# Kernel optimization log

Measured on AMD Instinct MI355X. Metric: run time of the kernel, lower is better.

## Reference

```python
import jax, jax.numpy as jnp
import numpy as np

N, E, D, L, G, C = 20000, 320000, 512, 6, 64, 10
EPS = 1e-5


def setup_inputs() -> dict:
    key = jax.random.key(0)
    ks = jax.random.split(key, 8)
    s = 0.05  # small init scale to keep activations sane across 6 layers
    x = jax.random.normal(ks[0], (N, D), jnp.float32)
    edge_index = jax.random.randint(ks[1], (2, E), 0, N, jnp.int32)
    batch = jnp.sort(jax.random.randint(ks[2], (N,), 0, G, jnp.int32))
    W_rel = jax.random.normal(ks[3], (L, D, D), jnp.float32) * s
    b_rel = jnp.zeros((L, D), jnp.float32)
    W_root = jax.random.normal(ks[4], (L, D, D), jnp.float32) * s
    gamma = jnp.ones((L, D), jnp.float32)
    beta = jnp.zeros((L, D), jnp.float32)
    lin_w = jax.random.normal(ks[5], (D, C), jnp.float32) * s
    lin_b = jnp.zeros((C,), jnp.float32)
    return {"x": x, "edge_index": edge_index, "batch": batch,
            "W_rel": W_rel, "b_rel": b_rel, "W_root": W_root,
            "gamma": gamma, "beta": beta, "lin_w": lin_w, "lin_b": lin_b}


def reference(x, edge_index, batch, W_rel, b_rel, W_root, gamma, beta, lin_w, lin_b):
    # PyG GraphConv (aggr='add'): out = segment_sum(x[src] -> dst) @ W_rel + b_rel + x @ W_root
    src, dst = edge_index[0], edge_index[1]
    n = x.shape[0]
    for l in range(W_rel.shape[0]):  # 6 structurally identical layers
        agg = jax.ops.segment_sum(x[src], dst, num_segments=n)  # [N, D]
        h = agg @ W_rel[l] + b_rel[l] + x @ W_root[l]
        # BatchNorm1d in training mode: biased batch statistics over nodes
        mu = jnp.mean(h, axis=0)
        var = jnp.mean(jnp.square(h - mu), axis=0)
        x = jax.nn.relu((h - mu) * jax.lax.rsqrt(var + EPS) * gamma[l] + beta[l])
    # global_mean_pool over per-node graph ids
    sums = jax.ops.segment_sum(x, batch, num_segments=G)              # [G, D]
    counts = jax.ops.segment_sum(jnp.ones((n,), x.dtype), batch, num_segments=G)
    pooled = sums / jnp.maximum(counts, 1.0)[:, None]
    return pooled @ lin_w + lin_b  # [G, C]
```

## Files before the change

kernel.cpp:

```cpp
#include <hip/hip_runtime.h>


typedef unsigned short u16;
typedef unsigned int u32;
typedef __attribute__((ext_vector_type(8))) short bf16x8;
typedef __attribute__((ext_vector_type(16))) float f32x16;

#define DFEAT 512
#define KDIM 1024
#define NLAYER 6
#define NGRAPH 64
#define NCLS 10
#define BN_EPS 1e-5f

__device__ __forceinline__ float bf_lo(u32 u) { union { u32 i; float f; } v; v.i = u << 16; return v.f; }
__device__ __forceinline__ float bf_hi(u32 u) { union { u32 i; float f; } v; v.i = u & 0xFFFF0000u; return v.f; }
__device__ __forceinline__ u16 f2bf(float f) {
  union { float f; u32 i; } v; v.f = f;
  u32 r = v.i + 0x7FFFu + ((v.i >> 16) & 1u);
  return (u16)(r >> 16);
}
__device__ __forceinline__ u32 pack2(float lo, float hi) {
  return (u32)f2bf(lo) | ((u32)f2bf(hi) << 16);
}

__device__ __forceinline__ void gload_lds16(const u16* g, u16* lds_base) {
  __builtin_amdgcn_global_load_lds(
      (const __attribute__((address_space(1))) u32*)g,
      (__attribute__((address_space(3))) u32*)lds_base, 16, 0, 0);
}

__global__ void prep_kernel(const int* __restrict__ ei, int* __restrict__ counts, int E,
                            const float* __restrict__ Wrel, const float* __restrict__ Wroot,
                            u16* __restrict__ Wt,
                            const float* __restrict__ x, u16* __restrict__ A, int M,
                            int histB, int wtB) {
  __shared__ float T[64][65];
  int b = blockIdx.x;
  if (b < histB) {
    int e = b * 256 + threadIdx.x;
    if (e < E) atomicAdd(&counts[ei[E + e]], 1);
  } else if (b < histB + wtB) {
    int t = b - histB;
    int nt = t & 7;
    int kt = (t >> 3) & 15;
    int l = t >> 7;
    int k0 = kt * 64, n0 = nt * 64;
    int tx = threadIdx.x & 63;
    int ty = threadIdx.x >> 6;
    const float* Wsrc = (k0 < DFEAT) ? (Wrel + ((size_t)l * DFEAT + k0) * DFEAT)
                                     : (Wroot + ((size_t)l * DFEAT + (k0 - DFEAT)) * DFEAT);
#pragma unroll
    for (int i = 0; i < 16; i++) {
      int ky = i * 4 + ty;
      T[ky][tx] = Wsrc[(size_t)ky * DFEAT + n0 + tx];
    }
    __syncthreads();
    u16* Wd = Wt + (size_t)l * DFEAT * KDIM + (size_t)n0 * KDIM + k0;
#pragma unroll
    for (int i = 0; i < 16; i++) {
      int ny = i * 4 + ty;
      Wd[(size_t)ny * KDIM + tx] = f2bf(T[tx][ny]);
    }
  } else {
    int idx = (b - histB - wtB) * 256 + threadIdx.x;
    int row = idx >> 7;
    int c4 = (idx & 127) * 4;
    if (row < M) {
      float4 v = *(const float4*)&x[(size_t)row * DFEAT + c4];
      uint2 o; o.x = pack2(v.x, v.y); o.y = pack2(v.z, v.w);
      *(uint2*)&A[(size_t)row * KDIM + DFEAT + c4] = o;
    }
  }
}

#define SCHUNK 20
__global__ __launch_bounds__(1024) void scan_kernel(const int* __restrict__ counts,
                                                    int* __restrict__ row_ptr,
                                                    int* __restrict__ cursor, int n) {
  __shared__ int part[1024];
  int tid = threadIdx.x;
  int base = tid * SCHUNK;
  int loc[SCHUNK];
  int s = 0;
#pragma unroll
  for (int i = 0; i < SCHUNK; i++) {
    int idx = base + i;
    int v = (idx < n) ? counts[idx] : 0;
    loc[i] = s; s += v;
  }
  part[tid] = s;
  __syncthreads();
  int x = s;
  for (int off = 1; off < 1024; off <<= 1) {
    int t = (tid >= off) ? part[tid - off] : 0;
    __syncthreads();
    x += t;
    part[tid] = x;
    __syncthreads();
  }
  int offset = x - s;
#pragma unroll
  for (int i = 0; i < SCHUNK; i++) {
    int idx = base + i;
    if (idx < n) { int v = offset + loc[i]; row_ptr[idx] = v; cursor[idx] = v; }
  }
  if (tid == 1023) row_ptr[n] = offset + s;
}

__global__ void scatter_kernel(const int* __restrict__ ei, int* __restrict__ cursor,
                               int* __restrict__ csr_src, int E) {
  int e = blockIdx.x * 256 + threadIdx.x;
  if (e < E) {
    int d = ei[E + e];
    int pos = atomicAdd(&cursor[d], 1);
    csr_src[pos] = ei[e];
  }
}

__device__ __forceinline__ void add8(uint4 v, float2* a) {
  a[0] += make_float2(bf_lo(v.x), bf_hi(v.x));
  a[1] += make_float2(bf_lo(v.y), bf_hi(v.y));
  a[2] += make_float2(bf_lo(v.z), bf_hi(v.z));
  a[3] += make_float2(bf_lo(v.w), bf_hi(v.w));
}

#define GCAP 1536
__global__ __launch_bounds__(256) void gather_kernel(u16* __restrict__ A,
                                                     const int* __restrict__ row_ptr,
                                                     const int* __restrict__ csr_src, int n) {
  __shared__ int sidx[GCAP];
  int b = blockIdx.x;
  int slice = b & 7;
  int grp = b >> 3;
  int tid = threadIdx.x;
  int r0 = grp * 32;
  int rend = (r0 + 32 < n) ? (r0 + 32) : n;
  int wbeg = row_ptr[r0], wend = row_ptr[rend];
  int cnt = wend - wbeg;
  bool lds_ok = (cnt <= GCAP);
  if (lds_ok)
    for (int t = tid; t < cnt; t += 256) sidx[t] = csr_src[wbeg + t];
  __syncthreads();

  int wid = tid >> 6, lane = tid & 63;
  int dsub = lane >> 3, fl = lane & 7;
  int dst = r0 + wid * 8 + dsub;
  if (dst >= n) return;
  int cc = slice * 64 + fl * 8;
  const u16* Sx = A + DFEAT + cc;
  int db = row_ptr[dst], de = row_ptr[dst + 1];
  float2 a[4] = {};
  if (lds_ok) {
    int e = db - wbeg, ee = de - wbeg;
    for (; e + 7 < ee; e += 8) {
      int s0 = sidx[e + 0], s1 = sidx[e + 1], s2 = sidx[e + 2], s3 = sidx[e + 3];
      int s4 = sidx[e + 4], s5 = sidx[e + 5], s6 = sidx[e + 6], s7 = sidx[e + 7];
      uint4 v0 = *(const uint4*)&Sx[(size_t)s0 * KDIM];
      uint4 v1 = *(const uint4*)&Sx[(size_t)s1 * KDIM];
      uint4 v2 = *(const uint4*)&Sx[(size_t)s2 * KDIM];
      uint4 v3 = *(const uint4*)&Sx[(size_t)s3 * KDIM];
      uint4 v4 = *(const uint4*)&Sx[(size_t)s4 * KDIM];
      uint4 v5 = *(const uint4*)&Sx[(size_t)s5 * KDIM];
      uint4 v6 = *(const uint4*)&Sx[(size_t)s6 * KDIM];
      uint4 v7 = *(const uint4*)&Sx[(size_t)s7 * KDIM];
      add8(v0, a); add8(v1, a); add8(v2, a); add8(v3, a);
      add8(v4, a); add8(v5, a); add8(v6, a); add8(v7, a);
    }
    for (; e < ee; ++e) {
      uint4 v = *(const uint4*)&Sx[(size_t)sidx[e] * KDIM];
      add8(v, a);
    }
  } else {
    for (int e = db; e < de; ++e) {
      uint4 v = *(const uint4*)&Sx[(size_t)csr_src[e] * KDIM];
      add8(v, a);
    }
  }
  uint4 o;
  o.x = pack2(a[0].x, a[0].y); o.y = pack2(a[1].x, a[1].y);
  o.z = pack2(a[2].x, a[2].y); o.w = pack2(a[3].x, a[3].y);
  *(uint4*)&A[(size_t)dst * KDIM + cc] = o;
}

#define BM 128
#define BN 128
#define BK 64
#define CSTR 132
__global__ __launch_bounds__(256, 4) void gemm_kernel(const u16* __restrict__ A,
                                                      const u16* __restrict__ Bt,
                                                      const float* __restrict__ bias,
                                                      u16* __restrict__ Hb,
                                                      float* __restrict__ sums, int M) {
  const int lin = blockIdx.x;
  const int bx = ((lin >> 5) << 3) + (lin & 7);
  const int by = (lin >> 3) & 3;
  const int m0 = bx * BM;
  if (m0 >= M) return;
  const int n0 = by * BN;

  __shared__ u16 smem[BM * CSTR];
  __shared__ float sred[2 * BN];
  u16* As = smem;
  u16* Bs = smem + BM * BK;
  const int tid = threadIdx.x;
  const int wid = tid >> 6, lane = tid & 63;
  const int wm = wid >> 1, wn = wid & 1;
  const int l31 = lane & 31, half = lane >> 5;

  if (tid < 2 * BN) sred[tid] = 0.f;

  const int dr = lane >> 3;
  const int gcol = ((lane & 7) ^ dr) * 8;
  int arow[4], brow[4];
#pragma unroll
  for (int t = 0; t < 4; t++) {
    int r = wid * 32 + t * 8 + dr;
    int ar = m0 + r; if (ar >= M) ar = M - 1;
    arow[t] = ar;
    brow[t] = n0 + r;
  }

  f32x16 acc[2][2] = {};

  for (int k0 = 0; k0 < KDIM; k0 += BK) {
    __syncthreads();
#pragma unroll
    for (int t = 0; t < 4; t++)
      gload_lds16(&A[(size_t)arow[t] * KDIM + k0 + gcol], &As[(wid * 32 + t * 8) * BK]);
#pragma unroll
    for (int t = 0; t < 4; t++)
      gload_lds16(&Bt[(size_t)brow[t] * KDIM + k0 + gcol], &Bs[(wid * 32 + t * 8) * BK]);
    __syncthreads();
#pragma unroll
    for (int ks = 0; ks < 4; ks++) {
      int slot = ((ks * 2 + half) ^ (l31 & 7)) * 8;
      bf16x8 a0 = *(const bf16x8*)&As[(wm * 64 + l31) * BK + slot];
      bf16x8 a1 = *(const bf16x8*)&As[(wm * 64 + 32 + l31) * BK + slot];
      bf16x8 b0 = *(const bf16x8*)&Bs[(wn * 64 + l31) * BK + slot];
      bf16x8 b1 = *(const bf16x8*)&Bs[(wn * 64 + 32 + l31) * BK + slot];
      acc[0][0] = __builtin_amdgcn_mfma_f32_32x32x16_bf16(a0, b0, acc[0][0], 0, 0, 0);
      acc[0][1] = __builtin_amdgcn_mfma_f32_32x32x16_bf16(a0, b1, acc[0][1], 0, 0, 0);
      acc[1][0] = __builtin_amdgcn_mfma_f32_32x32x16_bf16(a1, b0, acc[1][0], 0, 0, 0);
      acc[1][1] = __builtin_amdgcn_mfma_f32_32x32x16_bf16(a1, b1, acc[1][1], 0, 0, 0);
    }
  }

  __syncthreads();

#pragma unroll
  for (int nt = 0; nt < 2; nt++) {
    int colt = wn * 64 + nt * 32 + l31;
    float bv = bias[n0 + colt];
    float s = 0.f, s2 = 0.f;
#pragma unroll
    for (int mt = 0; mt < 2; mt++) {
      int rbase = wm * 64 + mt * 32 + half * 4;
#pragma unroll
      for (int reg = 0; reg < 16; reg++) {
        int rowt = rbase + (reg & 3) + 8 * (reg >> 2);
        float v = acc[mt][nt][reg] + bv;
        smem[rowt * CSTR + colt] = f2bf(v);
        if (m0 + rowt < M) { s += v; s2 += v * v; }
      }
    }
    s  += __shfl_xor(s, 32);
    s2 += __shfl_xor(s2, 32);
    if (half == 0) {
      atomicAdd(&sred[colt], s);
      atomicAdd(&sred[BN + colt], s2);
    }
  }
  __syncthreads();

  const int rsub = tid >> 4;
  const int c8 = (tid & 15) * 8;
#pragma unroll
  for (int it = 0; it < 8; it++) {
    int rowt = it * 16 + rsub;
    int grow = m0 + rowt;
    if (grow < M) {
      uint4 v = *(const uint4*)&smem[rowt * CSTR + c8];
      *(uint4*)&Hb[(size_t)grow * DFEAT + n0 + c8] = v;
    }
  }
  if (tid < BN) {
    atomicAdd(&sums[n0 + tid], sred[tid]);
    atomicAdd(&sums[DFEAT + n0 + tid], sred[BN + tid]);
  }
}

__global__ void norm_kernel(const u16* __restrict__ Hb, const float* __restrict__ sums,
                            const float* __restrict__ gamma, const float* __restrict__ beta,
                            u16* __restrict__ A, int M, float invN) {
  int idx = blockIdx.x * 256 + threadIdx.x;
  int row = idx >> 6;
  int c8 = (idx & 63) * 8;
  if (row >= M) return;
  float sc[8], sh[8];
#pragma unroll
  for (int j = 0; j < 8; j++) {
    int c = c8 + j;
    float mu = sums[c] * invN;
    float var = sums[DFEAT + c] * invN - mu * mu;
    float s = gamma[c] * rsqrtf(var + BN_EPS);
    sc[j] = s;
    sh[j] = beta[c] - mu * s;
  }
  uint4 h = *(const uint4*)&Hb[(size_t)row * DFEAT + c8];
  float x0 = fmaxf(bf_lo(h.x) * sc[0] + sh[0], 0.f);
  float x1 = fmaxf(bf_hi(h.x) * sc[1] + sh[1], 0.f);
  float x2 = fmaxf(bf_lo(h.y) * sc[2] + sh[2], 0.f);
  float x3 = fmaxf(bf_hi(h.y) * sc[3] + sh[3], 0.f);
  float x4 = fmaxf(bf_lo(h.z) * sc[4] + sh[4], 0.f);
  float x5 = fmaxf(bf_hi(h.z) * sc[5] + sh[5], 0.f);
  float x6 = fmaxf(bf_lo(h.w) * sc[6] + sh[6], 0.f);
  float x7 = fmaxf(bf_hi(h.w) * sc[7] + sh[7], 0.f);
  uint4 o; o.x = pack2(x0, x1); o.y = pack2(x2, x3);
  o.z = pack2(x4, x5); o.w = pack2(x6, x7);
  *(uint4*)&A[(size_t)row * KDIM + DFEAT + c8] = o;
}

__device__ __forceinline__ int lower_bound_dev(const int* a, int n, int v) {
  int lo = 0, hi = n;
  while (lo < hi) { int mid = (lo + hi) >> 1; if (a[mid] < v) lo = mid + 1; else hi = mid; }
  return lo;
}

__global__ __launch_bounds__(1024) void pool_kernel(const u16* __restrict__ Hb,
                                                    const float* __restrict__ sums,
                                                    const float* __restrict__ gamma,
                                                    const float* __restrict__ beta,
                                                    const int* __restrict__ batch,
                                                    float* __restrict__ pooled, int n, float invN) {
  __shared__ float red[DFEAT];
  int g = blockIdx.x;
  int tid = threadIdx.x;
  if (tid < DFEAT) red[tid] = 0.f;
  int lo = lower_bound_dev(batch, n, g);
  int hi = lower_bound_dev(batch, n, g + 1);
  int rowOff = tid >> 6, lane = tid & 63;
  int c0 = lane * 8;
  float sc[8], sh[8];
#pragma unroll
  for (int j = 0; j < 8; j++) {
    int c = c0 + j;
    float mu = sums[c] * invN;
    float var = sums[DFEAT + c] * invN - mu * mu;
    float s = gamma[c] * rsqrtf(var + BN_EPS);
    sc[j] = s;
    sh[j] = beta[c] - mu * s;
  }
  float a[8] = {};
  for (int r = lo + rowOff; r < hi; r += 16) {
    uint4 v = *(const uint4*)&Hb[(size_t)r * DFEAT + c0];
    float e0 = bf_lo(v.x), e1 = bf_hi(v.x), e2 = bf_lo(v.y), e3 = bf_hi(v.y);
    float e4 = bf_lo(v.z), e5 = bf_hi(v.z), e6 = bf_lo(v.w), e7 = bf_hi(v.w);
    a[0] += fmaxf(e0 * sc[0] + sh[0], 0.f); a[1] += fmaxf(e1 * sc[1] + sh[1], 0.f);
    a[2] += fmaxf(e2 * sc[2] + sh[2], 0.f); a[3] += fmaxf(e3 * sc[3] + sh[3], 0.f);
    a[4] += fmaxf(e4 * sc[4] + sh[4], 0.f); a[5] += fmaxf(e5 * sc[5] + sh[5], 0.f);
    a[6] += fmaxf(e6 * sc[6] + sh[6], 0.f); a[7] += fmaxf(e7 * sc[7] + sh[7], 0.f);
  }
  __syncthreads();
#pragma unroll
  for (int j = 0; j < 8; j++) atomicAdd(&red[c0 + j], a[j]);
  __syncthreads();
  if (tid < DFEAT) pooled[g * DFEAT + tid] = red[tid] / fmaxf((float)(hi - lo), 1.0f);
}

__global__ __launch_bounds__(64) void final_kernel(const float* __restrict__ pooled,
                                                   const float* __restrict__ lin_w,
                                                   const float* __restrict__ lin_b,
                                                   float* __restrict__ out) {
  int g = blockIdx.x;
  int lane = threadIdx.x;
  float acc[NCLS] = {};
  float4 p0 = *(const float4*)&pooled[g * DFEAT + lane * 8];
  float4 p1 = *(const float4*)&pooled[g * DFEAT + lane * 8 + 4];
  float pv[8] = {p0.x, p0.y, p0.z, p0.w, p1.x, p1.y, p1.z, p1.w};
#pragma unroll
  for (int j = 0; j < 8; j++) {
    int k = lane * 8 + j;
#pragma unroll
    for (int c = 0; c < NCLS; c++) acc[c] += pv[j] * lin_w[k * NCLS + c];
  }
#pragma unroll
  for (int off = 32; off > 0; off >>= 1)
#pragma unroll
    for (int c = 0; c < NCLS; c++) acc[c] += __shfl_down(acc[c], off);
  if (lane == 0)
#pragma unroll
    for (int c = 0; c < NCLS; c++) out[g * NCLS + c] = acc[c] + lin_b[c];
}

extern "C" void kernel_launch(void* const* d_in, const int* in_sizes, int n_in,
                              void* d_out, int out_size, void* d_ws, size_t ws_size,
                              hipStream_t stream) {
  const float* x      = (const float*)d_in[0];
  const int*   ei     = (const int*)d_in[1];
  const int*   batch  = (const int*)d_in[2];
  const float* W_rel  = (const float*)d_in[3];
  const float* b_rel  = (const float*)d_in[4];
  const float* W_root = (const float*)d_in[5];
  const float* gamma  = (const float*)d_in[6];
  const float* beta   = (const float*)d_in[7];
  const float* lin_w  = (const float*)d_in[8];
  const float* lin_b  = (const float*)d_in[9];
  float* out = (float*)d_out;

  const int N = in_sizes[0] / DFEAT;
  const int E = in_sizes[1] / 2;

  char* p = (char*)d_ws;
  u16*   A       = (u16*)p;    p += (size_t)N * KDIM * 2;
  u16*   Hb      = (u16*)p;    p += (size_t)N * DFEAT * 2;
  u16*   Wt      = (u16*)p;    p += (size_t)NLAYER * DFEAT * KDIM * 2;
  int*   row_ptr = (int*)p;    p += ((size_t)(N + 1) * 4 + 15) / 16 * 16;
  int*   cursor  = (int*)p;    p += (size_t)N * 4;
  int*   csr_src = (int*)p;    p += (size_t)E * 4;
  float* sums    = (float*)p;  p += (size_t)NLAYER * 2 * DFEAT * 4;
  float* pooled  = (float*)p;  p += (size_t)NGRAPH * DFEAT * 4;

  const float invN = 1.0f / (float)N;

  hipMemsetAsync(cursor, 0, (size_t)N * 4, stream);
  hipMemsetAsync(sums, 0, (size_t)NLAYER * 2 * DFEAT * 4, stream);

  const int histB = (E + 255) / 256;
  const int wtB = NLAYER * 16 * 8;
  const int xB = (N * 128 + 255) / 256;
  prep_kernel<<<histB + wtB + xB, 256, 0, stream>>>(ei, cursor, E, W_rel, W_root, Wt,
                                                    x, A, N, histB, wtB);
  scan_kernel<<<1, 1024, 0, stream>>>(cursor, row_ptr, cursor, N);
  scatter_kernel<<<(E + 255) / 256, 256, 0, stream>>>(ei, cursor, csr_src, E);

  const int ngrp8 = ((N + 31) / 32) * 8;
  const int gtiles = (((N + BM - 1) / BM + 7) / 8) * 8 * 4;

  for (int l = 0; l < NLAYER; ++l) {
    float* sums_l = sums + (size_t)l * 2 * DFEAT;
    gather_kernel<<<ngrp8, 256, 0, stream>>>(A, row_ptr, csr_src, N);
    gemm_kernel<<<gtiles, 256, 0, stream>>>(A, Wt + (size_t)l * DFEAT * KDIM,
                                            b_rel + (size_t)l * DFEAT, Hb, sums_l, N);
    if (l < NLAYER - 1)
      norm_kernel<<<(N * 64 + 255) / 256, 256, 0, stream>>>(
          Hb, sums_l, gamma + (size_t)l * DFEAT, beta + (size_t)l * DFEAT, A, N, invN);
  }

  pool_kernel<<<NGRAPH, 1024, 0, stream>>>(Hb, sums + (size_t)(NLAYER - 1) * 2 * DFEAT,
                                           gamma + (size_t)(NLAYER - 1) * DFEAT,
                                           beta + (size_t)(NLAYER - 1) * DFEAT,
                                           batch, pooled, N, invN);
  final_kernel<<<NGRAPH, 64, 0, stream>>>(pooled, lin_w, lin_b, out);
}
```

Baseline: 607.3 us.

## Unroll gather by 16, fuse final linear into pool, merge memsets

Adds a 16-wide unrolled loop to the edge gather so more independent row loads are in flight per wave. Folds the final classifier matmul into the pooling kernel using wave shuffles and LDS atomics, which removes one launch and the pooled buffer. Places the sums buffer next to cursor so a single memset clears both. The costs are higher register pressure in the gather and atomic ordering differences in the output reduction.

```diff
diff --git a/kernel.cpp b/kernel.cpp
--- a/kernel.cpp
+++ b/kernel.cpp
@@ -153,6 +153,32 @@
   float2 a[4] = {};
   if (lds_ok) {
     int e = db - wbeg, ee = de - wbeg;
+    for (; e + 15 < ee; e += 16) {
+      int s0 = sidx[e + 0], s1 = sidx[e + 1], s2 = sidx[e + 2], s3 = sidx[e + 3];
+      int s4 = sidx[e + 4], s5 = sidx[e + 5], s6 = sidx[e + 6], s7 = sidx[e + 7];
+      int s8 = sidx[e + 8], s9 = sidx[e + 9], sa = sidx[e + 10], sb = sidx[e + 11];
+      int sc_ = sidx[e + 12], sd = sidx[e + 13], se = sidx[e + 14], sf = sidx[e + 15];
+      uint4 v0 = *(const uint4*)&Sx[(size_t)s0 * KDIM];
+      uint4 v1 = *(const uint4*)&Sx[(size_t)s1 * KDIM];
+      uint4 v2 = *(const uint4*)&Sx[(size_t)s2 * KDIM];
+      uint4 v3 = *(const uint4*)&Sx[(size_t)s3 * KDIM];
+      uint4 v4 = *(const uint4*)&Sx[(size_t)s4 * KDIM];
+      uint4 v5 = *(const uint4*)&Sx[(size_t)s5 * KDIM];
+      uint4 v6 = *(const uint4*)&Sx[(size_t)s6 * KDIM];
+      uint4 v7 = *(const uint4*)&Sx[(size_t)s7 * KDIM];
+      uint4 v8 = *(const uint4*)&Sx[(size_t)s8 * KDIM];
+      uint4 v9 = *(const uint4*)&Sx[(size_t)s9 * KDIM];
+      uint4 va = *(const uint4*)&Sx[(size_t)sa * KDIM];
+      uint4 vb = *(const uint4*)&Sx[(size_t)sb * KDIM];
+      uint4 vc = *(const uint4*)&Sx[(size_t)sc_ * KDIM];
+      uint4 vd = *(const uint4*)&Sx[(size_t)sd * KDIM];
+      uint4 ve = *(const uint4*)&Sx[(size_t)se * KDIM];
+      uint4 vf = *(const uint4*)&Sx[(size_t)sf * KDIM];
+      add8(v0, a); add8(v1, a); add8(v2, a); add8(v3, a);
+      add8(v4, a); add8(v5, a); add8(v6, a); add8(v7, a);
+      add8(v8, a); add8(v9, a); add8(va, a); add8(vb, a);
+      add8(vc, a); add8(vd, a); add8(ve, a); add8(vf, a);
+    }
     for (; e + 7 < ee; e += 8) {
       int s0 = sidx[e + 0], s1 = sidx[e + 1], s2 = sidx[e + 2], s3 = sidx[e + 3];
       int s4 = sidx[e + 4], s5 = sidx[e + 5], s6 = sidx[e + 6], s7 = sidx[e + 7];
@@ -332,11 +358,15 @@
                                                     const float* __restrict__ gamma,
                                                     const float* __restrict__ beta,
                                                     const int* __restrict__ batch,
-                                                    float* __restrict__ pooled, int n, float invN) {
+                                                    const float* __restrict__ lin_w,
+                                                    const float* __restrict__ lin_b,
+                                                    float* __restrict__ out, int n, float invN) {
   __shared__ float red[DFEAT];
+  __shared__ float outred[NCLS];
   int g = blockIdx.x;
   int tid = threadIdx.x;
   if (tid < DFEAT) red[tid] = 0.f;
+  if (tid < NCLS) outred[tid] = 0.f;
   int lo = lower_bound_dev(batch, n, g);
   int hi = lower_bound_dev(batch, n, g + 1);
   int rowOff = tid >> 6, lane = tid & 63;
@@ -365,32 +395,19 @@
 #pragma unroll
   for (int j = 0; j < 8; j++) atomicAdd(&red[c0 + j], a[j]);
   __syncthreads();
-  if (tid < DFEAT) pooled[g * DFEAT + tid] = red[tid] / fmaxf((float)(hi - lo), 1.0f);
-}
-
-__global__ __launch_bounds__(64) void final_kernel(const float* __restrict__ pooled,
-                                                   const float* __restrict__ lin_w,
-                                                   const float* __restrict__ lin_b,
-                                                   float* __restrict__ out) {
-  int g = blockIdx.x;
-  int lane = threadIdx.x;
-  float acc[NCLS] = {};
-  float4 p0 = *(const float4*)&pooled[g * DFEAT + lane * 8];
-  float4 p1 = *(const float4*)&pooled[g * DFEAT + lane * 8 + 4];
-  float pv[8] = {p0.x, p0.y, p0.z, p0.w, p1.x, p1.y, p1.z, p1.w};
-#pragma unroll
-  for (int j = 0; j < 8; j++) {
-    int k = lane * 8 + j;
-#pragma unroll
-    for (int c = 0; c < NCLS; c++) acc[c] += pv[j] * lin_w[k * NCLS + c];
-  }
-#pragma unroll
-  for (int off = 32; off > 0; off >>= 1)
-#pragma unroll
-    for (int c = 0; c < NCLS; c++) acc[c] += __shfl_down(acc[c], off);
-  if (lane == 0)
-#pragma unroll
-    for (int c = 0; c < NCLS; c++) out[g * NCLS + c] = acc[c] + lin_b[c];
+  float invCnt = 1.0f / fmaxf((float)(hi - lo), 1.0f);
+  if (tid < DFEAT) {
+    float pk = red[tid] * invCnt;
+#pragma unroll
+    for (int c = 0; c < NCLS; c++) {
+      float v = pk * lin_w[tid * NCLS + c];
+#pragma unroll
+      for (int off = 32; off > 0; off >>= 1) v += __shfl_down(v, off);
+      if (lane == 0) atomicAdd(&outred[c], v);
+    }
+  }
+  __syncthreads();
+  if (tid < NCLS) out[g * NCLS + tid] = outred[tid] + lin_b[tid];
 }
 
 extern "C" void kernel_launch(void* const* d_in, const int* in_sizes, int n_in,
@@ -417,14 +434,12 @@
   u16*   Wt      = (u16*)p;    p += (size_t)NLAYER * DFEAT * KDIM * 2;
   int*   row_ptr = (int*)p;    p += ((size_t)(N + 1) * 4 + 15) / 16 * 16;
   int*   cursor  = (int*)p;    p += (size_t)N * 4;
+  float* sums    = (float*)p;  p += (size_t)NLAYER * 2 * DFEAT * 4;
   int*   csr_src = (int*)p;    p += (size_t)E * 4;
-  float* sums    = (float*)p;  p += (size_t)NLAYER * 2 * DFEAT * 4;
-  float* pooled  = (float*)p;  p += (size_t)NGRAPH * DFEAT * 4;
 
   const float invN = 1.0f / (float)N;
 
-  hipMemsetAsync(cursor, 0, (size_t)N * 4, stream);
-  hipMemsetAsync(sums, 0, (size_t)NLAYER * 2 * DFEAT * 4, stream);
+  hipMemsetAsync(cursor, 0, (size_t)N * 4 + (size_t)NLAYER * 2 * DFEAT * 4, stream);
 
   const int histB = (E + 255) / 256;
   const int wtB = NLAYER * 16 * 8;
@@ -450,6 +465,5 @@
   pool_kernel<<<NGRAPH, 1024, 0, stream>>>(Hb, sums + (size_t)(NLAYER - 1) * 2 * DFEAT,
                                            gamma + (size_t)(NLAYER - 1) * DFEAT,
                                            beta + (size_t)(NLAYER - 1) * DFEAT,
-                                           batch, pooled, N, invN);
-  final_kernel<<<NGRAPH, 64, 0, stream>>>(pooled, lin_w, lin_b, out);
-}
+                                           batch, lin_w, lin_b, out, N, invN);
+}
```

New measurement: 610.0 us. Within noise of the previous version (+0.4%).
